# Kernel optimization log

Measured on AMD Instinct MI355X. Metric: run time of the kernel, lower is better.

The kernel has to match this reference:

```python
import jax, jax.numpy as jnp
import numpy as np

EPS = 1e-8  # torch CosineSimilarity default eps

def setup_inputs() -> dict:
    key = jax.random.key(0)
    kv, kt, k1, k2, k3, k4 = jax.random.split(key, 6)
    B, S = 16, 1024
    VD, TD, H = 1024, 768, 512
    visual_features = jax.random.normal(kv, (B, S, VD), dtype=jnp.float32)
    text_features = jax.random.normal(kt, (B, S, TD), dtype=jnp.float32)
    # nn.Linear params: weight [out, in], bias [out]
    Wv = jax.random.normal(k1, (H, VD), dtype=jnp.float32) * (1.0 / np.sqrt(VD))
    bv = jax.random.normal(k2, (H,), dtype=jnp.float32) * 0.01
    Wt = jax.random.normal(k3, (H, TD), dtype=jnp.float32) * (1.0 / np.sqrt(TD))
    bt = jax.random.normal(k4, (H,), dtype=jnp.float32) * 0.01
    return {"visual_features": visual_features, "text_features": text_features,
            "Wv": Wv, "bv": bv, "Wt": Wt, "bt": bt}

def reference(visual_features, text_features, Wv, bv, Wt, bt):
    # Linear projections
    v = jnp.einsum('bsd,hd->bsh', visual_features, Wv) + bv  # [B,S,H]
    t = jnp.einsum('bsd,hd->bsh', text_features, Wt) + bt    # [B,S,H]
    # Cosine similarity matrix via normalized batched GEMM
    # (algebraically equal to broadcasting CosineSimilarity over (B,S,S,H))
    dots = jnp.einsum('bih,bjh->bij', v, t)                   # [B,S,S]
    vn = jnp.linalg.norm(v, axis=-1)                          # [B,S]
    tn = jnp.linalg.norm(t, axis=-1)                          # [B,S]
    denom = jnp.maximum(vn[:, :, None] * tn[:, None, :], EPS)
    return dots / denom
```

## Files before the change

kernel.cpp:

```cpp
#include <hip/hip_runtime.h>
#include <hip/hip_bf16.h>

typedef __bf16 bf16x8 __attribute__((ext_vector_type(8)));
typedef __bf16 bf16x4 __attribute__((ext_vector_type(4)));
typedef float  f32x4  __attribute__((ext_vector_type(4)));

#define MFMA16(a, b, c) __builtin_amdgcn_mfma_f32_16x16x32_bf16((a), (b), (c), 0, 0, 0)

#define BATCH 16
#define SEQ   1024
#define VD    1024
#define TD    768
#define HDIM  512
#define MROWS (BATCH * SEQ)

typedef __attribute__((address_space(1))) const unsigned int gas_uint;
typedef __attribute__((address_space(3))) unsigned int las_uint;

__device__ __forceinline__ void async_copy16(const void* g, void* l) {
    __builtin_amdgcn_global_load_lds((gas_uint*)g, (las_uint*)l, 16, 0, 0);
}

__device__ __forceinline__ void stage_tile256(const __bf16* __restrict__ src,
                                              size_t ld, int row0, int k0,
                                              __bf16* __restrict__ buf, int tid) {
#pragma unroll
    for (int i = 0; i < 4; ++i) {
        const int c = i * 512 + tid;
        const int r = c >> 3;
        const int g = (c & 7) ^ (r & 7);
        async_copy16(&src[(size_t)(row0 + r) * ld + k0 + g * 8],
                     &buf[(c & ~63) * 8]);
    }
}

__device__ __forceinline__ bf16x8 frag_read(const __bf16* __restrict__ buf,
                                            int r, int h, int fq) {
    return *reinterpret_cast<const bf16x8*>(&buf[(r * 8 + ((h * 4 + fq) ^ (r & 7))) * 8]);
}

#define NC_XV (BATCH * SEQ * VD / 4)
#define NC_XT (BATCH * SEQ * TD / 4)
#define NC_WV (HDIM * VD / 4)
#define NC_WT (HDIM * TD / 4)
#define NC_TOTAL (NC_XV + NC_XT + NC_WV + NC_WT)
#define NPAIRS (NC_TOTAL / 2)
#define CONV_PAIR_BLOCKS (NPAIRS / 256)
#define NZ4 (2 * MROWS / 4)
#define NZ_BLOCKS (NZ4 / 256)
#define CONV_GRID (CONV_PAIR_BLOCKS + NZ_BLOCKS)

__global__ __launch_bounds__(256) void conv_kernel(
    const float* __restrict__ Xv, const float* __restrict__ Xt,
    const float* __restrict__ Wv, const float* __restrict__ Wt,
    __bf16* __restrict__ Xvb, __bf16* __restrict__ Xtb,
    __bf16* __restrict__ Wvb, __bf16* __restrict__ Wtb,
    float* __restrict__ n2z) {
    const int blk = blockIdx.x;
    if (blk >= CONV_PAIR_BLOCKS) {
        const int zi = (blk - CONV_PAIR_BLOCKS) * 256 + threadIdx.x;
        reinterpret_cast<float4*>(n2z)[zi] = float4{0.f, 0.f, 0.f, 0.f};
        return;
    }
    int k = (blk * 256 + threadIdx.x) * 2;
    const float* src;
    __bf16* dst;
    if (k < NC_XV)                 { src = Xv; dst = Xvb; }
    else if ((k -= NC_XV) < NC_XT) { src = Xt; dst = Xtb; }
    else if ((k -= NC_XT) < NC_WV) { src = Wv; dst = Wvb; }
    else { k -= NC_WV;               src = Wt; dst = Wtb; }
    const float4 x0 = reinterpret_cast<const float4*>(src)[k];
    const float4 x1 = reinterpret_cast<const float4*>(src)[k + 1];
    bf16x8 q = {(__bf16)x0.x, (__bf16)x0.y, (__bf16)x0.z, (__bf16)x0.w,
                (__bf16)x1.x, (__bf16)x1.y, (__bf16)x1.z, (__bf16)x1.w};
    reinterpret_cast<bf16x8*>(dst)[k >> 1] = q;
}

__global__ __launch_bounds__(512, 2) void proj_kernel(
    const __bf16* __restrict__ Xvb, const __bf16* __restrict__ Wvb, const float* __restrict__ bv_,
    const __bf16* __restrict__ Xtb, const __bf16* __restrict__ Wtb, const float* __restrict__ bt_,
    __bf16* __restrict__ vout, __bf16* __restrict__ tout,
    float* __restrict__ vn2, float* __restrict__ tn2)
{
    __shared__ __bf16 As[2][256 * 64];
    __shared__ __bf16 Bs[2][256 * 64];

    const int L  = blockIdx.x;
    const int x  = L & 7;
    const int s  = L >> 3;
    const int z  = s >> 4;
    const int ss = s & 15;
    const int m0 = (x * 8 + (ss >> 1)) * 256;
    const int n0 = (ss & 1) * 256;

    const __bf16* X; const __bf16* Wb; const float* bias; __bf16* out; float* n2; int K;
    if (z == 0) { X = Xvb; Wb = Wvb; bias = bv_; out = vout; n2 = vn2; K = VD; }
    else        { X = Xtb; Wb = Wtb; bias = bt_; out = tout; n2 = tn2; K = TD; }

    const int tid  = threadIdx.x;
    const int lane = tid & 63;
    const int wave = tid >> 6;
    const int wr   = wave >> 2;
    const int wc   = wave & 3;
    const int fr   = lane & 15;
    const int fq   = lane >> 4;

    f32x4 acc[8][4] = {};
    const int NKT = K >> 6;

    stage_tile256(X,  K, m0, 0,  As[0], tid);
    stage_tile256(Wb, K, n0, 0,  Bs[0], tid);
    stage_tile256(X,  K, m0, 64, As[1], tid);
    stage_tile256(Wb, K, n0, 64, Bs[1], tid);
    asm volatile("s_waitcnt vmcnt(8)" ::: "memory");
    __builtin_amdgcn_s_barrier();

    for (int kt = 0; kt < NKT; ++kt) {
        const __bf16* Ab = As[kt & 1];
        const __bf16* Bb = Bs[kt & 1];
        bf16x8 bfr[4][2];
#pragma unroll
        for (int q = 0; q < 4; ++q) {
            bf16x8 afr[2][2];
#pragma unroll
            for (int m2 = 0; m2 < 2; ++m2)
#pragma unroll
                for (int h = 0; h < 2; ++h)
                    afr[m2][h] = frag_read(Ab, wr * 128 + (q * 2 + m2) * 16 + fr, h, fq);
            if (q == 0) {
#pragma unroll
                for (int n = 0; n < 4; ++n)
#pragma unroll
                    for (int h = 0; h < 2; ++h)
                        bfr[n][h] = frag_read(Bb, wc * 64 + n * 16 + fr, h, fq);
            }
            __builtin_amdgcn_s_barrier();
            __builtin_amdgcn_s_setprio(1);
#pragma unroll
            for (int h = 0; h < 2; ++h)
#pragma unroll
                for (int m2 = 0; m2 < 2; ++m2)
#pragma unroll
                    for (int n = 0; n < 4; ++n)
                        acc[q * 2 + m2][n] = MFMA16(afr[m2][h], bfr[n][h], acc[q * 2 + m2][n]);
            __builtin_amdgcn_s_setprio(0);
        }
        if (kt < NKT - 1) {
            __builtin_amdgcn_s_barrier();
            __builtin_amdgcn_sched_barrier(0);
            if (kt + 2 < NKT) {
                const int kk = (kt + 2) << 6;
                stage_tile256(X,  K, m0, kk, As[kt & 1], tid);
                stage_tile256(Wb, K, n0, kk, Bs[kt & 1], tid);
                asm volatile("s_waitcnt vmcnt(8)" ::: "memory");
            } else {
                asm volatile("s_waitcnt vmcnt(0)" ::: "memory");
            }
            __builtin_amdgcn_sched_barrier(0);
            __builtin_amdgcn_s_barrier();
        }
    }

    float bc[4];
#pragma unroll
    for (int n = 0; n < 4; ++n)
        bc[n] = bias[n0 + wc * 64 + n * 16 + fr];

#pragma unroll
    for (int mf = 0; mf < 8; ++mf) {
        const int rowb = m0 + wr * 128 + mf * 16 + fq * 4;
#pragma unroll
        for (int r = 0; r < 4; ++r) {
            float s_ = 0.f;
#pragma unroll
            for (int n = 0; n < 4; ++n) {
                const float e = acc[mf][n][r] + bc[n];
                out[(size_t)(rowb + r) * HDIM + n0 + wc * 64 + n * 16 + fr] = (__bf16)e;
                s_ = fmaf(e, e, s_);
            }
            s_ += __shfl_xor(s_, 1);
            s_ += __shfl_xor(s_, 2);
            s_ += __shfl_xor(s_, 4);
            s_ += __shfl_xor(s_, 8);
            if (fr == 0) atomicAdd(&n2[rowb + r], s_);
        }
    }
}

__global__ __launch_bounds__(512, 2) void dots_kernel(const __bf16* __restrict__ v,
                                                      const __bf16* __restrict__ t,
                                                      const float* __restrict__ vn2,
                                                      const float* __restrict__ tn2,
                                                      float* __restrict__ out) {
    __shared__ __bf16 As[2][256 * 64];
    __shared__ __bf16 Bs[2][256 * 64];

    const int L  = blockIdx.x;
    const int x  = L & 7;
    const int s  = L >> 3;
    const int b  = x * 2 + (s >> 4);
    const int i0 = ((s >> 2) & 3) * 256;
    const int j0 = (s & 3) * 256;

    const __bf16* vb = v + (size_t)b * SEQ * HDIM;
    const __bf16* tb = t + (size_t)b * SEQ * HDIM;

    const int tid  = threadIdx.x;
    const int lane = tid & 63;
    const int wave = tid >> 6;
    const int wr   = wave >> 2;
    const int wc   = wave & 3;
    const int fr   = lane & 15;
    const int fq   = lane >> 4;

    f32x4 acc[8][4] = {};
    const int NKT = HDIM >> 6;

    stage_tile256(vb, HDIM, i0, 0,  As[0], tid);
    stage_tile256(tb, HDIM, j0, 0,  Bs[0], tid);
    stage_tile256(vb, HDIM, i0, 64, As[1], tid);
    stage_tile256(tb, HDIM, j0, 64, Bs[1], tid);
    asm volatile("s_waitcnt vmcnt(8)" ::: "memory");
    __builtin_amdgcn_s_barrier();

    for (int kt = 0; kt < NKT; ++kt) {
        const __bf16* Ab = As[kt & 1];
        const __bf16* Bb = Bs[kt & 1];
        bf16x8 bfr[4][2];
#pragma unroll
        for (int q = 0; q < 4; ++q) {
            bf16x8 afr[2][2];
#pragma unroll
            for (int m2 = 0; m2 < 2; ++m2)
#pragma unroll
                for (int h = 0; h < 2; ++h)
                    afr[m2][h] = frag_read(Ab, wr * 128 + (q * 2 + m2) * 16 + fr, h, fq);
            if (q == 0) {
#pragma unroll
                for (int n = 0; n < 4; ++n)
#pragma unroll
                    for (int h = 0; h < 2; ++h)
                        bfr[n][h] = frag_read(Bb, wc * 64 + n * 16 + fr, h, fq);
            }
            __builtin_amdgcn_s_barrier();
            __builtin_amdgcn_s_setprio(1);
#pragma unroll
            for (int h = 0; h < 2; ++h)
#pragma unroll
                for (int m2 = 0; m2 < 2; ++m2)
#pragma unroll
                    for (int n = 0; n < 4; ++n)
                        acc[q * 2 + m2][n] = MFMA16(afr[m2][h], bfr[n][h], acc[q * 2 + m2][n]);
            __builtin_amdgcn_s_setprio(0);
        }
        if (kt < NKT - 1) {
            __builtin_amdgcn_s_barrier();
            __builtin_amdgcn_sched_barrier(0);
            if (kt + 2 < NKT) {
                const int kk = (kt + 2) << 6;
                stage_tile256(vb, HDIM, i0, kk, As[kt & 1], tid);
                stage_tile256(tb, HDIM, j0, kk, Bs[kt & 1], tid);
                asm volatile("s_waitcnt vmcnt(8)" ::: "memory");
            } else {
                asm volatile("s_waitcnt vmcnt(0)" ::: "memory");
            }
            __builtin_amdgcn_sched_barrier(0);
            __builtin_amdgcn_s_barrier();
        }
    }

    float vr2[8][4];
#pragma unroll
    for (int mf = 0; mf < 8; ++mf)
#pragma unroll
        for (int r = 0; r < 4; ++r)
            vr2[mf][r] = vn2[b * SEQ + i0 + wr * 128 + mf * 16 + fq * 4 + r];

    float* outb = out + ((size_t)b << 20);
#pragma unroll
    for (int n = 0; n < 4; ++n) {
        const int j     = j0 + wc * 64 + n * 16 + fr;
        const float tj2 = tn2[b * SEQ + j];
#pragma unroll
        for (int mf = 0; mf < 8; ++mf) {
            const int ib = i0 + wr * 128 + mf * 16 + fq * 4;
#pragma unroll
            for (int r = 0; r < 4; ++r) {
                const float denom = fmaxf(sqrtf(vr2[mf][r] * tj2), 1e-8f);
                outb[(size_t)(ib + r) * SEQ + j] = acc[mf][n][r] * __builtin_amdgcn_rcpf(denom);
            }
        }
    }
}

extern "C" void kernel_launch(void* const* d_in, const int* in_sizes, int n_in,
                              void* d_out, int out_size, void* d_ws, size_t ws_size,
                              hipStream_t stream) {
    const float* Xv = (const float*)d_in[0];
    const float* Xt = (const float*)d_in[1];
    const float* Wv = (const float*)d_in[2];
    const float* bv = (const float*)d_in[3];
    const float* Wt = (const float*)d_in[4];
    const float* bt = (const float*)d_in[5];
    float* out = (float*)d_out;

    char* ws = (char*)d_ws;
    size_t off = 0;
    __bf16* v   = (__bf16*)(ws + off); off += (size_t)MROWS * HDIM * 2;
    __bf16* t   = (__bf16*)(ws + off); off += (size_t)MROWS * HDIM * 2;
    __bf16* Xvb = (__bf16*)(ws + off); off += (size_t)MROWS * VD * 2;
    __bf16* Xtb = (__bf16*)(ws + off); off += (size_t)MROWS * TD * 2;
    __bf16* Wvb = (__bf16*)(ws + off); off += (size_t)HDIM * VD * 2;
    __bf16* Wtb = (__bf16*)(ws + off); off += (size_t)HDIM * TD * 2;
    float*  vn2 = (float*)(ws + off);  off += (size_t)MROWS * 4;
    float*  tn2 = (float*)(ws + off);  off += (size_t)MROWS * 4;

    conv_kernel<<<CONV_GRID, 256, 0, stream>>>(Xv, Xt, Wv, Wt, Xvb, Xtb, Wvb, Wtb, vn2);

    proj_kernel<<<256, 512, 0, stream>>>(Xvb, Wvb, bv, Xtb, Wtb, bt, v, t, vn2, tn2);

    dots_kernel<<<256, 512, 0, stream>>>(v, t, vn2, tn2, out);
}
```

Baseline: 242.9 us.

## Fuse fp32-to-bf16 activation conversion into projection GEMM A-tile staging

The projection kernel now loads fp32 activations straight into registers, converts them to bf16 and writes them to swizzled LDS. This replaces the separate conversion pass over the activations and the bf16 copies it wrote to workspace. The change removes one full read and write of the large activation tensors through HBM. In exchange, the A-tile loads go through registers instead of async global-to-LDS copies, which raises register pressure and adds conversion ALU work and LDS-store waits inside the GEMM pipeline.

```diff
diff --git a/kernel.cpp b/kernel.cpp
--- a/kernel.cpp
+++ b/kernel.cpp
@@ -39,36 +39,56 @@
     return *reinterpret_cast<const bf16x8*>(&buf[(r * 8 + ((h * 4 + fq) ^ (r & 7))) * 8]);
 }
 
-#define NC_XV (BATCH * SEQ * VD / 4)
-#define NC_XT (BATCH * SEQ * TD / 4)
+__device__ __forceinline__ void ldA_f32(const float* __restrict__ src, int K,
+                                        int row0, int k0, int tid, float4* regs) {
+#pragma unroll
+    for (int i = 0; i < 4; ++i) {
+        const int c = i * 512 + tid;
+        const int r = c >> 3;
+        const int j = c & 7;
+        const float4* p = reinterpret_cast<const float4*>(src) +
+                          (size_t)(row0 + r) * (K >> 2) + (k0 >> 2) + j * 2;
+        regs[i * 2]     = p[0];
+        regs[i * 2 + 1] = p[1];
+    }
+}
+
+__device__ __forceinline__ void stA_lds(__bf16* __restrict__ buf, int tid,
+                                        const float4* regs) {
+#pragma unroll
+    for (int i = 0; i < 4; ++i) {
+        const int c = i * 512 + tid;
+        const int r = c >> 3;
+        const int j = c & 7;
+        const float4 x0 = regs[i * 2], x1 = regs[i * 2 + 1];
+        bf16x8 q = {(__bf16)x0.x, (__bf16)x0.y, (__bf16)x0.z, (__bf16)x0.w,
+                    (__bf16)x1.x, (__bf16)x1.y, (__bf16)x1.z, (__bf16)x1.w};
+        *reinterpret_cast<bf16x8*>(&buf[(r * 8 + (j ^ (r & 7))) * 8]) = q;
+    }
+}
+
 #define NC_WV (HDIM * VD / 4)
 #define NC_WT (HDIM * TD / 4)
-#define NC_TOTAL (NC_XV + NC_XT + NC_WV + NC_WT)
-#define NPAIRS (NC_TOTAL / 2)
-#define CONV_PAIR_BLOCKS (NPAIRS / 256)
-#define NZ4 (2 * MROWS / 4)
-#define NZ_BLOCKS (NZ4 / 256)
-#define CONV_GRID (CONV_PAIR_BLOCKS + NZ_BLOCKS)
-
-__global__ __launch_bounds__(256) void conv_kernel(
-    const float* __restrict__ Xv, const float* __restrict__ Xt,
+#define NW_PAIRS ((NC_WV + NC_WT) / 2)
+#define CONVW_BLOCKS (NW_PAIRS / 256)
+#define NZ_BLOCKS (2 * MROWS / 4 / 256)
+#define CONVW_GRID (CONVW_BLOCKS + NZ_BLOCKS)
+
+__global__ __launch_bounds__(256) void conv_w_kernel(
     const float* __restrict__ Wv, const float* __restrict__ Wt,
-    __bf16* __restrict__ Xvb, __bf16* __restrict__ Xtb,
     __bf16* __restrict__ Wvb, __bf16* __restrict__ Wtb,
     float* __restrict__ n2z) {
     const int blk = blockIdx.x;
-    if (blk >= CONV_PAIR_BLOCKS) {
-        const int zi = (blk - CONV_PAIR_BLOCKS) * 256 + threadIdx.x;
+    if (blk >= CONVW_BLOCKS) {
+        const int zi = (blk - CONVW_BLOCKS) * 256 + threadIdx.x;
         reinterpret_cast<float4*>(n2z)[zi] = float4{0.f, 0.f, 0.f, 0.f};
         return;
     }
     int k = (blk * 256 + threadIdx.x) * 2;
     const float* src;
     __bf16* dst;
-    if (k < NC_XV)                 { src = Xv; dst = Xvb; }
-    else if ((k -= NC_XV) < NC_XT) { src = Xt; dst = Xtb; }
-    else if ((k -= NC_XT) < NC_WV) { src = Wv; dst = Wvb; }
-    else { k -= NC_WV;               src = Wt; dst = Wtb; }
+    if (k < NC_WV) { src = Wv; dst = Wvb; }
+    else { k -= NC_WV; src = Wt; dst = Wtb; }
     const float4 x0 = reinterpret_cast<const float4*>(src)[k];
     const float4 x1 = reinterpret_cast<const float4*>(src)[k + 1];
     bf16x8 q = {(__bf16)x0.x, (__bf16)x0.y, (__bf16)x0.z, (__bf16)x0.w,
@@ -77,8 +97,8 @@
 }
 
 __global__ __launch_bounds__(512, 2) void proj_kernel(
-    const __bf16* __restrict__ Xvb, const __bf16* __restrict__ Wvb, const float* __restrict__ bv_,
-    const __bf16* __restrict__ Xtb, const __bf16* __restrict__ Wtb, const float* __restrict__ bt_,
+    const float* __restrict__ Xv32, const __bf16* __restrict__ Wvb, const float* __restrict__ bv_,
+    const float* __restrict__ Xt32, const __bf16* __restrict__ Wtb, const float* __restrict__ bt_,
     __bf16* __restrict__ vout, __bf16* __restrict__ tout,
     float* __restrict__ vn2, float* __restrict__ tn2)
 {
@@ -93,9 +113,9 @@
     const int m0 = (x * 8 + (ss >> 1)) * 256;
     const int n0 = (ss & 1) * 256;
 
-    const __bf16* X; const __bf16* Wb; const float* bias; __bf16* out; float* n2; int K;
-    if (z == 0) { X = Xvb; Wb = Wvb; bias = bv_; out = vout; n2 = vn2; K = VD; }
-    else        { X = Xtb; Wb = Wtb; bias = bt_; out = tout; n2 = tn2; K = TD; }
+    const float* X; const __bf16* Wb; const float* bias; __bf16* out; float* n2; int K;
+    if (z == 0) { X = Xv32; Wb = Wvb; bias = bv_; out = vout; n2 = vn2; K = VD; }
+    else        { X = Xt32; Wb = Wtb; bias = bt_; out = tout; n2 = tn2; K = TD; }
 
     const int tid  = threadIdx.x;
     const int lane = tid & 63;
@@ -108,14 +128,25 @@
     f32x4 acc[8][4] = {};
     const int NKT = K >> 6;
 
-    stage_tile256(X,  K, m0, 0,  As[0], tid);
-    stage_tile256(Wb, K, n0, 0,  Bs[0], tid);
-    stage_tile256(X,  K, m0, 64, As[1], tid);
-    stage_tile256(Wb, K, n0, 64, Bs[1], tid);
-    asm volatile("s_waitcnt vmcnt(8)" ::: "memory");
-    __builtin_amdgcn_s_barrier();
-
+    {
+        float4 rA0[8], rA1[8];
+        ldA_f32(X, K, m0, 0,  tid, rA0);
+        ldA_f32(X, K, m0, 64, tid, rA1);
+        stage_tile256(Wb, K, n0, 0,  Bs[0], tid);
+        stage_tile256(Wb, K, n0, 64, Bs[1], tid);
+        stA_lds(As[0], tid, rA0);
+        stA_lds(As[1], tid, rA1);
+        asm volatile("s_waitcnt vmcnt(4)" ::: "memory");
+        asm volatile("s_waitcnt lgkmcnt(0)" ::: "memory");
+        __builtin_amdgcn_s_barrier();
+    }
+
+    float4 regs[8];
     for (int kt = 0; kt < NKT; ++kt) {
+        if (kt + 2 < NKT) {
+            ldA_f32(X, K, m0, (kt + 2) << 6, tid, regs);
+            __builtin_amdgcn_sched_barrier(0);
+        }
         const __bf16* Ab = As[kt & 1];
         const __bf16* Bb = Bs[kt & 1];
         bf16x8 bfr[4][2];
@@ -149,13 +180,13 @@
             __builtin_amdgcn_s_barrier();
             __builtin_amdgcn_sched_barrier(0);
             if (kt + 2 < NKT) {
-                const int kk = (kt + 2) << 6;
-                stage_tile256(X,  K, m0, kk, As[kt & 1], tid);
-                stage_tile256(Wb, K, n0, kk, Bs[kt & 1], tid);
-                asm volatile("s_waitcnt vmcnt(8)" ::: "memory");
+                stA_lds(As[kt & 1], tid, regs);
+                stage_tile256(Wb, K, n0, (kt + 2) << 6, Bs[kt & 1], tid);
+                asm volatile("s_waitcnt vmcnt(4)" ::: "memory");
             } else {
                 asm volatile("s_waitcnt vmcnt(0)" ::: "memory");
             }
+            asm volatile("s_waitcnt lgkmcnt(0)" ::: "memory");
             __builtin_amdgcn_sched_barrier(0);
             __builtin_amdgcn_s_barrier();
         }
@@ -308,16 +339,14 @@
     size_t off = 0;
     __bf16* v   = (__bf16*)(ws + off); off += (size_t)MROWS * HDIM * 2;
     __bf16* t   = (__bf16*)(ws + off); off += (size_t)MROWS * HDIM * 2;
-    __bf16* Xvb = (__bf16*)(ws + off); off += (size_t)MROWS * VD * 2;
-    __bf16* Xtb = (__bf16*)(ws + off); off += (size_t)MROWS * TD * 2;
     __bf16* Wvb = (__bf16*)(ws + off); off += (size_t)HDIM * VD * 2;
     __bf16* Wtb = (__bf16*)(ws + off); off += (size_t)HDIM * TD * 2;
     float*  vn2 = (float*)(ws + off);  off += (size_t)MROWS * 4;
     float*  tn2 = (float*)(ws + off);  off += (size_t)MROWS * 4;
 
-    conv_kernel<<<CONV_GRID, 256, 0, stream>>>(Xv, Xt, Wv, Wt, Xvb, Xtb, Wvb, Wtb, vn2);
-
-    proj_kernel<<<256, 512, 0, stream>>>(Xvb, Wvb, bv, Xtb, Wtb, bt, v, t, vn2, tn2);
+    conv_w_kernel<<<CONVW_GRID, 256, 0, stream>>>(Wv, Wt, Wvb, Wtb, vn2);
+
+    proj_kernel<<<256, 512, 0, stream>>>(Xv, Wvb, bv, Xt, Wtb, bt, v, t, vn2, tn2);
 
     dots_kernel<<<256, 512, 0, stream>>>(v, t, vn2, tn2, out);
 }
```

Measured after the change: 236.9 us. 2.5% less time.
